# Kernel tuning notes

Hardware: AMD Instinct MI355X
Metric: run time of the kernel (lower is better)

The kernel has to match this reference:

```python
import jax, jax.numpy as jnp
import numpy as np

B, L, T, IN, H, OUT = 1024, 64, 128, 13, 64, 13
NEG = -1e30


def gru_step(x, h, Wih, Whh, bih, bhh):
    # PyTorch GRU cell: gates ordered (r, z, n)
    gi = x @ Wih.T + bih          # [B, 3H]
    gh = h @ Whh.T + bhh          # [B, 3H]
    ir, iz, inn = jnp.split(gi, 3, axis=-1)
    hr, hz, hn = jnp.split(gh, 3, axis=-1)
    r = jax.nn.sigmoid(ir + hr)
    z = jax.nn.sigmoid(iz + hz)
    n = jnp.tanh(inn + r * hn)
    return (1.0 - z) * n + z * h


def setup_inputs() -> dict:
    key = jax.random.key(0)
    ks = jax.random.split(key, 10)
    s = float(1.0 / np.sqrt(H))
    x = jax.random.normal(ks[0], (B, L, IN), jnp.float32)
    lengths = jax.random.randint(ks[1], (B,), 1, L + 1).at[0].set(L)
    Wih = jax.random.uniform(ks[2], (3 * H, IN), jnp.float32, -s, s)
    Whh = jax.random.uniform(ks[3], (3 * H, H), jnp.float32, -s, s)
    bih = jax.random.uniform(ks[4], (3 * H,), jnp.float32, -s, s)
    bhh = jax.random.uniform(ks[5], (3 * H,), jnp.float32, -s, s)
    Wf = jax.random.uniform(ks[6], (OUT, H), jnp.float32, -s, s)
    bf = jax.random.uniform(ks[7], (OUT,), jnp.float32, -s, s)
    Wa = jax.random.uniform(ks[8], (H, H), jnp.float32, -s, s)
    ba = jax.random.uniform(ks[9], (H,), jnp.float32, -s, s)
    return dict(x=x, lengths=lengths, output_length=T, Wih=Wih, Whh=Whh,
                bih=bih, bhh=bhh, Wf=Wf, bf=bf, Wa=Wa, ba=ba)


def reference(x, lengths, output_length, Wih, Whh, bih, bhh, Wf, bf, Wa, ba):
    b, l = x.shape[0], x.shape[1]
    xT = jnp.swapaxes(x, 0, 1)                        # [L, B, IN]
    h0 = jnp.zeros((b, H), x.dtype)

    # Encoder: masked GRU emulating pack_padded/pad_packed semantics:
    # hidden frozen past each sequence's length; outputs zero past length.
    def enc(h, inp):
        t, xt = inp
        hn = gru_step(xt, h, Wih, Whh, bih, bhh)
        valid = (t < lengths)[:, None]
        h = jnp.where(valid, hn, h)
        return h, jnp.where(valid, hn, 0.0)

    h, outs = jax.lax.scan(enc, h0, (jnp.arange(l), xT))
    # output[:, -1, :] of the padded output (zeros for seqs shorter than max)
    nin = outs[-1] @ Wf.T + bf                        # [B, OUT]

    Tn = output_length
    buf0 = jnp.zeros((Tn, b, H), x.dtype)             # growing past-prediction buffer

    def dec(carry, t):
        h, buf, nin = carry
        hn = gru_step(nin, h, Wih, Whh, bih, bhh)     # output_lstm == hidden (1 layer, 1 step)
        # attention recomputed over all past predictions (softmax over time axis)
        logits = jnp.einsum('tbh,gh->tbg', buf, Wa) + ba      # [T, B, H]
        logits = jnp.where((jnp.arange(Tn) < t)[:, None, None], logits, NEG)
        w = jax.nn.softmax(logits, axis=0)
        o = hn + jnp.sum(w * buf, axis=0)             # at t=0 buffer is all zeros -> +0
        y = o @ Wf.T + bf
        return (hn, buf.at[t].set(o), y), y

    _, ys = jax.lax.scan(dec, (h, buf0, nin), jnp.arange(Tn))
    return jnp.swapaxes(ys, 0, 1)                     # [B, T, OUT]
```

## Files before the change

kernel.cpp:

```cpp
#include <hip/hip_runtime.h>
#include <stdint.h>
#include <math.h>

#define BATCH 1024
#define SEQL  64
#define TDEC  128
#define NIN   13
#define NH    64
#define NOUT  13

typedef _Float16 h2 __attribute__((ext_vector_type(2)));
typedef __fp16   g2 __attribute__((ext_vector_type(2)));

union FU  { uint32_t u; float f; };
union HU  { uint16_t u; _Float16 h; };
union H2U { uint32_t u; h2 h; g2 g; };

__device__ __forceinline__ float bf2f(uint16_t v) { FU t; t.u = ((uint32_t)v) << 16; return t.f; }
__device__ __forceinline__ float hf2f(uint16_t v) { HU t; t.u = v; return (float)t.h; }

__device__ __forceinline__ float ldf(const void* p, long i, int mode) {
    if (mode == 1) return bf2f(((const uint16_t*)p)[i]);
    if (mode == 2) return hf2f(((const uint16_t*)p)[i]);
    return ((const float*)p)[i];
}

__device__ __forceinline__ bool pass_stats(const void* p, int n, int lane, int mode,
                                           float band_lo, float band_hi, float max_ok) {
    int m = (n + 1) / 2;
    int cnt = (m < 64) ? m : 64;
    bool ok_max = true, in_band = false;
    if (lane < cnt) {
        long pos = 2L * (((long)lane * m) / cnt);
        float v = (mode == 1) ? bf2f(((const uint16_t*)p)[pos])
                              : hf2f(((const uint16_t*)p)[pos]);
        float a = fabsf(v);
        ok_max  = (a <= max_ok);
        in_band = (a >= band_lo && a <= band_hi);
    }
    bool allmax = __all(ok_max);
    int nb = (int)__popcll(__ballot(in_band));
    int need = cnt / 4; if (need < 1) need = 1;
    return allmax && (nb >= need);
}
__device__ __forceinline__ int detect(const void* p, int n, int lane,
                                      float band_lo, float band_hi, float max_ok) {
    if (pass_stats(p, n, lane, 1, band_lo, band_hi, max_ok)) return 1;
    if (pass_stats(p, n, lane, 2, band_lo, band_hi, max_ok)) return 2;
    return 0;
}
__device__ __forceinline__ bool detect_len64(const int* p, int lane) {
    int v = p[2 * lane + 1];
    return __all(v == 0);
}

__device__ __forceinline__ float dot2(h2 a, h2 b, float c) {
#if __has_builtin(__builtin_amdgcn_fdot2)
    return __builtin_amdgcn_fdot2(a, b, c, false);
#else
    return c + (float)a[0] * (float)b[0] + (float)a[1] * (float)b[1];
#endif
}
__device__ __forceinline__ uint32_t pku(float a, float b) {
    H2U t; t.g = __builtin_amdgcn_cvt_pkrtz(a, b); return t.u;
}
__device__ __forceinline__ h2 uh(uint32_t u) { H2U t; t.u = u; return t.h; }
__device__ __forceinline__ float rcp_(float x) { return __builtin_amdgcn_rcpf(x); }
__device__ __forceinline__ float exp2_(float x) {
#if __has_builtin(__builtin_amdgcn_exp2f)
    return __builtin_amdgcn_exp2f(x);
#else
    return __expf(x * 0.69314718056f);
#endif
}
__device__ __forceinline__ float sigm2(float xs)  { return rcp_(1.0f + exp2_(-xs)); }
__device__ __forceinline__ float tanh2(float xs)  { return 1.0f - 2.0f * rcp_(exp2_(xs) + 1.0f); }
__device__ __forceinline__ void wb() { __builtin_amdgcn_wave_barrier(); }

__device__ __forceinline__ float swap1(float v) {
    FU a; a.f = v;
    FU b; b.u = (uint32_t)__builtin_amdgcn_mov_dpp((int)a.u, 0xB1, 0xF, 0xF, true);
    return b.f;
}

#define BWRITE(DSTB, V)                                                    \
    {                                                                      \
        float _w  = swap1(V);                                              \
        float _lo = odd ? _w  : (V);                                       \
        float _hi = odd ? (V) : _w;                                        \
        (DSTB)[jhalf] = pku(_lo, _hi);                                     \
    }

#define BREAD(SRC, DST)                                                    \
    {                                                                      \
        _Pragma("unroll")                                                  \
        for (int _k = 0; _k < 32; _k += 4) {                               \
            uint4 _q = *(const uint4*)((SRC) + _k);                        \
            (DST)[_k]     = _q.x; (DST)[_k + 1] = _q.y;                    \
            (DST)[_k + 2] = _q.z; (DST)[_k + 3] = _q.w;                    \
        }                                                                  \
    }

#define DEC_STEP(T_, HRD, HWR, OB_, YSLOT)                                         \
    {                                                                              \
        uint32_t hpk[32];                                                          \
        BREAD(HRD, hpk);                                                           \
        float arA = bcr, azA = bcz, hnA = bnh, anA = bni;                          \
        float arB = 0.0f, azB = 0.0f, hnB = 0.0f;                                  \
        float arC = 0.0f, azC = 0.0f, hnC = 0.0f;                                  \
        float arD = 0.0f, azD = 0.0f, hnD = 0.0f;                                  \
        _Pragma("unroll")                                                          \
        for (int k = 0; k < 32; k += 4) {                                          \
            h2 h0 = uh(hpk[k]), h1 = uh(hpk[k + 1]);                               \
            h2 h2v = uh(hpk[k + 2]), h3 = uh(hpk[k + 3]);                          \
            arA = dot2(whhr[k],     h0, arA); azA = dot2(whhz[k],     h0, azA); hnA = dot2(whhn[k],     h0, hnA); \
            arB = dot2(whhr[k + 1], h1, arB); azB = dot2(whhz[k + 1], h1, azB); hnB = dot2(whhn[k + 1], h1, hnB); \
            arC = dot2(whhr[k + 2], h2v, arC); azC = dot2(whhz[k + 2], h2v, azC); hnC = dot2(whhn[k + 2], h2v, hnC); \
            arD = dot2(whhr[k + 3], h3, arD); azD = dot2(whhz[k + 3], h3, azD); hnD = dot2(whhn[k + 3], h3, hnD); \
        }                                                                          \
        _Pragma("unroll")                                                          \
        for (int p = 0; p < 7; ++p) {                                              \
            h2 xv = uh(ypk[p]);                                                    \
            arB = dot2(wihr[p], xv, arB);                                          \
            azB = dot2(wihz[p], xv, azB);                                          \
            anA = dot2(wihn[p], xv, anA);                                          \
        }                                                                          \
        float ar = (arA + arB) + (arC + arD);                                      \
        float az = (azA + azB) + (azC + azD);                                      \
        float hna = (hnA + hnB) + (hnC + hnD);                                     \
        float r_ = sigm2(ar);                                                      \
        float z_ = sigm2(az);                                                      \
        float n_ = tanh2(anA + r_ * hna);                                          \
        float hnew = n_ + z_ * (h - n_);                                           \
        h = hnew;                                                                  \
        BWRITE(HWR, hnew);                                                         \
        float attn = ((T_) > 0) ? num * rcp_(Zs) : 0.0f;                           \
        float o_ = hnew + attn;                                                    \
        BWRITE(OB_, o_);                                                           \
        uint32_t opk[32];                                                          \
        BREAD(OB_, opk);                                                           \
        float sA = baj, yA = bfj, sB = 0.0f, yB = 0.0f;                            \
        float sC = 0.0f, yC = 0.0f, sD = 0.0f, yD = 0.0f;                          \
        _Pragma("unroll")                                                          \
        for (int k = 0; k < 32; k += 4) {                                          \
            h2 o0 = uh(opk[k]), o1 = uh(opk[k + 1]);                               \
            h2 o2 = uh(opk[k + 2]), o3 = uh(opk[k + 3]);                           \
            sA = dot2(wap[k],     o0, sA); yA = dot2(wfp[k],     o0, yA);          \
            sB = dot2(wap[k + 1], o1, sB); yB = dot2(wfp[k + 1], o1, yB);          \
            sC = dot2(wap[k + 2], o2, sC); yC = dot2(wfp[k + 2], o2, yC);          \
            sD = dot2(wap[k + 3], o3, sD); yD = dot2(wfp[k + 3], o3, yD);          \
        }                                                                          \
        float yv_ = (yA + yB) + (yC + yD);                                         \
        YSLOT = yv_;                                                               \
        float yz = (j < NOUT) ? yv_ : 0.0f;                                        \
        uint32_t pr_ = pku(yz, swap1(yz));                                         \
        _Pragma("unroll")                                                          \
        for (int k = 0; k < 7; ++k) ypk[k] = __builtin_amdgcn_readlane(pr_, 2 * k);\
        float s_  = (sA + sB) + (sC + sD);                                         \
        float mn = fmaxf(m, s_);                                                   \
        float al = exp2_(m - mn);                                                  \
        float pp = exp2_(s_ - mn);                                                 \
        Zs  = Zs * al + pp;                                                        \
        num = num * al + pp * o_;                                                  \
        m = mn;                                                                    \
    }

#define ENC_STEP(T_, HRD, HWR)                                                     \
    {                                                                              \
        uint32_t hpk[32];                                                          \
        BREAD(HRD, hpk);                                                           \
        uint4 q0 = *(const uint4*)(&xs2[(T_)][0]);                                 \
        uint4 q1 = *(const uint4*)(&xs2[(T_)][4]);                                 \
        float arA = bcr, azA = bcz, hnA = bnh, anA = bni;                          \
        float arB = 0.0f, azB = 0.0f, hnB = 0.0f;                                  \
        float arC = 0.0f, azC = 0.0f, hnC = 0.0f;                                  \
        float arD = 0.0f, azD = 0.0f, hnD = 0.0f;                                  \
        _Pragma("unroll")                                                          \
        for (int k = 0; k < 32; k += 4) {                                          \
            h2 h0 = uh(hpk[k]), h1 = uh(hpk[k + 1]);                               \
            h2 h2v = uh(hpk[k + 2]), h3 = uh(hpk[k + 3]);                          \
            arA = dot2(whhr[k],     h0, arA); azA = dot2(whhz[k],     h0, azA); hnA = dot2(whhn[k],     h0, hnA); \
            arB = dot2(whhr[k + 1], h1, arB); azB = dot2(whhz[k + 1], h1, azB); hnB = dot2(whhn[k + 1], h1, hnB); \
            arC = dot2(whhr[k + 2], h2v, arC); azC = dot2(whhz[k + 2], h2v, azC); hnC = dot2(whhn[k + 2], h2v, hnC); \
            arD = dot2(whhr[k + 3], h3, arD); azD = dot2(whhz[k + 3], h3, azD); hnD = dot2(whhn[k + 3], h3, hnD); \
        }                                                                          \
        {                                                                          \
            uint32_t xw[8] = {q0.x, q0.y, q0.z, q0.w, q1.x, q1.y, q1.z, q1.w};     \
            _Pragma("unroll")                                                      \
            for (int p = 0; p < 7; ++p) {                                          \
                h2 xv = uh(xw[p]);                                                 \
                arB = dot2(wihr[p], xv, arB);                                      \
                azB = dot2(wihz[p], xv, azB);                                      \
                anA = dot2(wihn[p], xv, anA);                                      \
            }                                                                      \
        }                                                                          \
        float ar = (arA + arB) + (arC + arD);                                      \
        float az = (azA + azB) + (azC + azD);                                      \
        float hna = (hnA + hnB) + (hnC + hnD);                                     \
        float r_ = sigm2(ar);                                                      \
        float z_ = sigm2(az);                                                      \
        float n_ = tanh2(anA + r_ * hna);                                          \
        float hnew = n_ + z_ * (h - n_);                                           \
        bool upd = ((T_) < len);                                                   \
        h = upd ? hnew : h;                                                        \
        if ((T_) == SEQL - 1) out_last = upd ? hnew : 0.0f;                        \
        BWRITE(HWR, h);                                                            \
    }

__global__ __launch_bounds__(64, 1)
void gru_attn_kernel(const void* __restrict__ x, const int* __restrict__ lengths,
                     const void* __restrict__ Wih, const void* __restrict__ Whh,
                     const void* __restrict__ bih, const void* __restrict__ bhh,
                     const void* __restrict__ Wf, const void* __restrict__ bfv,
                     const void* __restrict__ Wa, const void* __restrict__ ba,
                     float* __restrict__ out)
{
    const int b = blockIdx.x;
    const int j = threadIdx.x;
    const bool odd = j & 1;
    const int jhalf = j >> 1;

    __shared__ __align__(16) uint32_t xs2[SEQL][8];
    __shared__ __align__(16) uint32_t hb[2][32];
    __shared__ __align__(16) uint32_t ob[2][32];

    const int dX   = detect(x,   BATCH * SEQL * NIN, j, 0.25f, 4.0f, 16.0f);
    const int dWih = detect(Wih, 3 * NH * NIN, j, 0.04f, 0.13f, 0.14f);
    const int dWhh = detect(Whh, 3 * NH * NH,  j, 0.04f, 0.13f, 0.14f);
    const int dBih = detect(bih, 3 * NH,       j, 0.04f, 0.13f, 0.14f);
    const int dBhh = detect(bhh, 3 * NH,       j, 0.04f, 0.13f, 0.14f);
    const int dWf  = detect(Wf,  NOUT * NH,    j, 0.04f, 0.13f, 0.14f);
    const int dBf  = detect(bfv, NOUT,         j, 0.04f, 0.13f, 0.14f);
    const int dWa  = detect(Wa,  NH * NH,      j, 0.04f, 0.13f, 0.14f);
    const int dBa  = detect(ba,  NH,           j, 0.04f, 0.13f, 0.14f);
    const bool len64 = detect_len64(lengths, j);

    const float L2E  = 1.44269504089f;
    const float L2E2 = 2.88539008177f;

    h2 wihr[7], wihz[7], wihn[7];
    h2 whhr[32], whhz[32], whhn[32];
    h2 wap[32], wfp[32];

#pragma unroll
    for (int k = 0; k < 7; ++k) {
        float a0 = ldf(Wih, (0 * NH + j) * NIN + 2 * k, dWih);
        float a1 = (2 * k + 1 < NIN) ? ldf(Wih, (0 * NH + j) * NIN + 2 * k + 1, dWih) : 0.0f;
        wihr[k] = uh(pku(a0 * L2E, a1 * L2E));
        float b0 = ldf(Wih, (1 * NH + j) * NIN + 2 * k, dWih);
        float b1 = (2 * k + 1 < NIN) ? ldf(Wih, (1 * NH + j) * NIN + 2 * k + 1, dWih) : 0.0f;
        wihz[k] = uh(pku(b0 * L2E, b1 * L2E));
        float c0 = ldf(Wih, (2 * NH + j) * NIN + 2 * k, dWih);
        float c1 = (2 * k + 1 < NIN) ? ldf(Wih, (2 * NH + j) * NIN + 2 * k + 1, dWih) : 0.0f;
        wihn[k] = uh(pku(c0 * L2E2, c1 * L2E2));
    }
    const int jf = (j < NOUT) ? j : 0;
#pragma unroll
    for (int k = 0; k < 32; ++k) {
        whhr[k] = uh(pku(ldf(Whh, (0 * NH + j) * NH + 2 * k, dWhh) * L2E,
                         ldf(Whh, (0 * NH + j) * NH + 2 * k + 1, dWhh) * L2E));
        whhz[k] = uh(pku(ldf(Whh, (1 * NH + j) * NH + 2 * k, dWhh) * L2E,
                         ldf(Whh, (1 * NH + j) * NH + 2 * k + 1, dWhh) * L2E));
        whhn[k] = uh(pku(ldf(Whh, (2 * NH + j) * NH + 2 * k, dWhh) * L2E2,
                         ldf(Whh, (2 * NH + j) * NH + 2 * k + 1, dWhh) * L2E2));
        wap[k]  = uh(pku(ldf(Wa, j * NH + 2 * k, dWa) * L2E,
                         ldf(Wa, j * NH + 2 * k + 1, dWa) * L2E));
        wfp[k]  = uh(pku(ldf(Wf, jf * NH + 2 * k, dWf),
                         ldf(Wf, jf * NH + 2 * k + 1, dWf)));
    }

    const float bcr = (ldf(bih, j, dBih)      + ldf(bhh, j, dBhh))      * L2E;
    const float bcz = (ldf(bih, NH + j, dBih) + ldf(bhh, NH + j, dBhh)) * L2E;
    const float bni = ldf(bih, 2 * NH + j, dBih) * L2E2;
    const float bnh = ldf(bhh, 2 * NH + j, dBhh) * L2E2;
    const float baj = ldf(ba, j, dBa) * L2E;
    const float bfj = ldf(bfv, jf, dBf);
    const int len = len64 ? lengths[2 * b] : lengths[b];

    {
        const long base = ((long)b * SEQL + j) * NIN;
        float v[14];
#pragma unroll
        for (int k = 0; k < NIN; ++k) v[k] = ldf(x, base + k, dX);
        v[13] = 0.0f;
#pragma unroll
        for (int p = 0; p < 7; ++p) xs2[j][p] = pku(v[2 * p], v[2 * p + 1]);
        xs2[j][7] = 0u;
    }
    wb();

    float h = 0.0f;
    float out_last = 0.0f;

    BWRITE(&hb[0][0], 0.0f);

#pragma unroll 1
    for (int t0 = 0; t0 < SEQL; t0 += 2) {
        ENC_STEP(t0,     (&hb[0][0]), (&hb[1][0]));
        ENC_STEP(t0 + 1, (&hb[1][0]), (&hb[0][0]));
    }

    uint32_t ypk[7];
    {
        BWRITE(&ob[0][0], out_last);
        uint32_t opk[32];
        BREAD(&ob[0][0], opk);
        float nA = bfj, nB = 0.0f, nC = 0.0f, nD = 0.0f;
#pragma unroll
        for (int k = 0; k < 32; k += 4) {
            nA = dot2(wfp[k],     uh(opk[k]),     nA);
            nB = dot2(wfp[k + 1], uh(opk[k + 1]), nB);
            nC = dot2(wfp[k + 2], uh(opk[k + 2]), nC);
            nD = dot2(wfp[k + 3], uh(opk[k + 3]), nD);
        }
        float nv = (nA + nB) + (nC + nD);
        float nz = (j < NOUT) ? nv : 0.0f;
        uint32_t pr = pku(nz, swap1(nz));
#pragma unroll
        for (int k = 0; k < 7; ++k) ypk[k] = __builtin_amdgcn_readlane(pr, 2 * k);
    }

    float m = -1e30f, Zs = 0.0f, num = 0.0f;

#pragma unroll 1
    for (int t0 = 0; t0 < TDEC; t0 += 4) {
        float y0, y1, y2, y3;
        DEC_STEP(t0 + 0, (&hb[0][0]), (&hb[1][0]), (&ob[0][0]), y0);
        DEC_STEP(t0 + 1, (&hb[1][0]), (&hb[0][0]), (&ob[1][0]), y1);
        DEC_STEP(t0 + 2, (&hb[0][0]), (&hb[1][0]), (&ob[0][0]), y2);
        DEC_STEP(t0 + 3, (&hb[1][0]), (&hb[0][0]), (&ob[1][0]), y3);
        if (j < NOUT) {
            size_t base_ = ((size_t)b * TDEC + t0) * NOUT + j;
            out[base_]            = y0;
            out[base_ + NOUT]     = y1;
            out[base_ + 2 * NOUT] = y2;
            out[base_ + 3 * NOUT] = y3;
        }
    }
}

extern "C" void kernel_launch(void* const* d_in, const int* in_sizes, int n_in,
                              void* d_out, int out_size, void* d_ws, size_t ws_size,
                              hipStream_t stream) {
    (void)in_sizes; (void)n_in; (void)out_size; (void)d_ws; (void)ws_size;
    const void* x      = d_in[0];
    const int* lengths = (const int*)d_in[1];
    const void* Wih = d_in[3];
    const void* Whh = d_in[4];
    const void* bih = d_in[5];
    const void* bhh = d_in[6];
    const void* Wf  = d_in[7];
    const void* bf  = d_in[8];
    const void* Wa  = d_in[9];
    const void* ba  = d_in[10];
    float* out = (float*)d_out;

    gru_attn_kernel<<<dim3(BATCH), dim3(64), 0, stream>>>(
        x, lengths, Wih, Whh, bih, bhh, Wf, bf, Wa, ba, out);
}
```

Baseline: 210.3 us.

## Process two batch sequences per wavefront with interleaved independent recurrences

Each 64-lane block now handles two batch elements, interleaving the two independent GRU/attention recurrences so their dot-product chains can overlap and hide latency. This halves the grid to 512 blocks. Encoder inputs now stay in registers and are broadcast with readlane instead of being staged in shared memory. The cost is more register pressure and fewer blocks, which on a chip with many CUs may leave some units idle.

Result: slower. 308.4 us (+46.6%).

```diff
diff --git a/kernel.cpp b/kernel.cpp
--- a/kernel.cpp
+++ b/kernel.cpp
@@ -90,7 +90,6 @@
         float _hi = odd ? (V) : _w;                                        \
         (DSTB)[jhalf] = pku(_lo, _hi);                                     \
     }
-
 #define BREAD(SRC, DST)                                                    \
     {                                                                      \
         _Pragma("unroll")                                                  \
@@ -101,110 +100,73 @@
         }                                                                  \
     }
 
-#define DEC_STEP(T_, HRD, HWR, OB_, YSLOT)                                         \
-    {                                                                              \
-        uint32_t hpk[32];                                                          \
-        BREAD(HRD, hpk);                                                           \
-        float arA = bcr, azA = bcz, hnA = bnh, anA = bni;                          \
-        float arB = 0.0f, azB = 0.0f, hnB = 0.0f;                                  \
-        float arC = 0.0f, azC = 0.0f, hnC = 0.0f;                                  \
-        float arD = 0.0f, azD = 0.0f, hnD = 0.0f;                                  \
-        _Pragma("unroll")                                                          \
-        for (int k = 0; k < 32; k += 4) {                                          \
-            h2 h0 = uh(hpk[k]), h1 = uh(hpk[k + 1]);                               \
-            h2 h2v = uh(hpk[k + 2]), h3 = uh(hpk[k + 3]);                          \
-            arA = dot2(whhr[k],     h0, arA); azA = dot2(whhz[k],     h0, azA); hnA = dot2(whhn[k],     h0, hnA); \
-            arB = dot2(whhr[k + 1], h1, arB); azB = dot2(whhz[k + 1], h1, azB); hnB = dot2(whhn[k + 1], h1, hnB); \
-            arC = dot2(whhr[k + 2], h2v, arC); azC = dot2(whhz[k + 2], h2v, azC); hnC = dot2(whhn[k + 2], h2v, hnC); \
-            arD = dot2(whhr[k + 3], h3, arD); azD = dot2(whhz[k + 3], h3, azD); hnD = dot2(whhn[k + 3], h3, hnD); \
-        }                                                                          \
-        _Pragma("unroll")                                                          \
-        for (int p = 0; p < 7; ++p) {                                              \
-            h2 xv = uh(ypk[p]);                                                    \
-            arB = dot2(wihr[p], xv, arB);                                          \
-            azB = dot2(wihz[p], xv, azB);                                          \
-            anA = dot2(wihn[p], xv, anA);                                          \
-        }                                                                          \
-        float ar = (arA + arB) + (arC + arD);                                      \
-        float az = (azA + azB) + (azC + azD);                                      \
-        float hna = (hnA + hnB) + (hnC + hnD);                                     \
-        float r_ = sigm2(ar);                                                      \
-        float z_ = sigm2(az);                                                      \
-        float n_ = tanh2(anA + r_ * hna);                                          \
-        float hnew = n_ + z_ * (h - n_);                                           \
-        h = hnew;                                                                  \
-        BWRITE(HWR, hnew);                                                         \
-        float attn = ((T_) > 0) ? num * rcp_(Zs) : 0.0f;                           \
-        float o_ = hnew + attn;                                                    \
-        BWRITE(OB_, o_);                                                           \
-        uint32_t opk[32];                                                          \
-        BREAD(OB_, opk);                                                           \
-        float sA = baj, yA = bfj, sB = 0.0f, yB = 0.0f;                            \
-        float sC = 0.0f, yC = 0.0f, sD = 0.0f, yD = 0.0f;                          \
-        _Pragma("unroll")                                                          \
-        for (int k = 0; k < 32; k += 4) {                                          \
-            h2 o0 = uh(opk[k]), o1 = uh(opk[k + 1]);                               \
-            h2 o2 = uh(opk[k + 2]), o3 = uh(opk[k + 3]);                           \
-            sA = dot2(wap[k],     o0, sA); yA = dot2(wfp[k],     o0, yA);          \
-            sB = dot2(wap[k + 1], o1, sB); yB = dot2(wfp[k + 1], o1, yB);          \
-            sC = dot2(wap[k + 2], o2, sC); yC = dot2(wfp[k + 2], o2, yC);          \
-            sD = dot2(wap[k + 3], o3, sD); yD = dot2(wfp[k + 3], o3, yD);          \
-        }                                                                          \
-        float yv_ = (yA + yB) + (yC + yD);                                         \
-        YSLOT = yv_;                                                               \
-        float yz = (j < NOUT) ? yv_ : 0.0f;                                        \
-        uint32_t pr_ = pku(yz, swap1(yz));                                         \
-        _Pragma("unroll")                                                          \
-        for (int k = 0; k < 7; ++k) ypk[k] = __builtin_amdgcn_readlane(pr_, 2 * k);\
-        float s_  = (sA + sB) + (sC + sD);                                         \
-        float mn = fmaxf(m, s_);                                                   \
-        float al = exp2_(m - mn);                                                  \
-        float pp = exp2_(s_ - mn);                                                 \
-        Zs  = Zs * al + pp;                                                        \
-        num = num * al + pp * o_;                                                  \
-        m = mn;                                                                    \
-    }
-
-#define ENC_STEP(T_, HRD, HWR)                                                     \
-    {                                                                              \
-        uint32_t hpk[32];                                                          \
-        BREAD(HRD, hpk);                                                           \
-        uint4 q0 = *(const uint4*)(&xs2[(T_)][0]);                                 \
-        uint4 q1 = *(const uint4*)(&xs2[(T_)][4]);                                 \
-        float arA = bcr, azA = bcz, hnA = bnh, anA = bni;                          \
-        float arB = 0.0f, azB = 0.0f, hnB = 0.0f;                                  \
-        float arC = 0.0f, azC = 0.0f, hnC = 0.0f;                                  \
-        float arD = 0.0f, azD = 0.0f, hnD = 0.0f;                                  \
-        _Pragma("unroll")                                                          \
-        for (int k = 0; k < 32; k += 4) {                                          \
-            h2 h0 = uh(hpk[k]), h1 = uh(hpk[k + 1]);                               \
-            h2 h2v = uh(hpk[k + 2]), h3 = uh(hpk[k + 3]);                          \
-            arA = dot2(whhr[k],     h0, arA); azA = dot2(whhz[k],     h0, azA); hnA = dot2(whhn[k],     h0, hnA); \
-            arB = dot2(whhr[k + 1], h1, arB); azB = dot2(whhz[k + 1], h1, azB); hnB = dot2(whhn[k + 1], h1, hnB); \
-            arC = dot2(whhr[k + 2], h2v, arC); azC = dot2(whhz[k + 2], h2v, azC); hnC = dot2(whhn[k + 2], h2v, hnC); \
-            arD = dot2(whhr[k + 3], h3, arD); azD = dot2(whhz[k + 3], h3, azD); hnD = dot2(whhn[k + 3], h3, hnD); \
-        }                                                                          \
-        {                                                                          \
-            uint32_t xw[8] = {q0.x, q0.y, q0.z, q0.w, q1.x, q1.y, q1.z, q1.w};     \
-            _Pragma("unroll")                                                      \
-            for (int p = 0; p < 7; ++p) {                                          \
-                h2 xv = uh(xw[p]);                                                 \
-                arB = dot2(wihr[p], xv, arB);                                      \
-                azB = dot2(wihz[p], xv, azB);                                      \
-                anA = dot2(wihn[p], xv, anA);                                      \
-            }                                                                      \
-        }                                                                          \
-        float ar = (arA + arB) + (arC + arD);                                      \
-        float az = (azA + azB) + (azC + azD);                                      \
-        float hna = (hnA + hnB) + (hnC + hnD);                                     \
-        float r_ = sigm2(ar);                                                      \
-        float z_ = sigm2(az);                                                      \
-        float n_ = tanh2(anA + r_ * hna);                                          \
-        float hnew = n_ + z_ * (h - n_);                                           \
-        bool upd = ((T_) < len);                                                   \
-        h = upd ? hnew : h;                                                        \
-        if ((T_) == SEQL - 1) out_last = upd ? hnew : 0.0f;                        \
-        BWRITE(HWR, h);                                                            \
+#define DECL_ACC(S)                                                        \
+    float arA##S = bcr, azA##S = bcz, hnA##S = bnh, anA##S = bni;          \
+    float arB##S = 0.0f, azB##S = 0.0f, hnB##S = 0.0f;                     \
+    float arC##S = 0.0f, azC##S = 0.0f, hnC##S = 0.0f;                     \
+    float arD##S = 0.0f, azD##S = 0.0f, hnD##S = 0.0f;
+
+#define WHHQ(S, k)                                                         \
+    {                                                                      \
+        h2 q0 = uh(hpk##S[(k)]),     q1 = uh(hpk##S[(k) + 1]);             \
+        h2 q2 = uh(hpk##S[(k) + 2]), q3 = uh(hpk##S[(k) + 3]);             \
+        arA##S = dot2(whhr[(k)],     q0, arA##S); azA##S = dot2(whhz[(k)],     q0, azA##S); hnA##S = dot2(whhn[(k)],     q0, hnA##S); \
+        arB##S = dot2(whhr[(k) + 1], q1, arB##S); azB##S = dot2(whhz[(k) + 1], q1, azB##S); hnB##S = dot2(whhn[(k) + 1], q1, hnB##S); \
+        arC##S = dot2(whhr[(k) + 2], q2, arC##S); azC##S = dot2(whhz[(k) + 2], q2, azC##S); hnC##S = dot2(whhn[(k) + 2], q2, hnC##S); \
+        arD##S = dot2(whhr[(k) + 3], q3, arD##S); azD##S = dot2(whhz[(k) + 3], q3, azD##S); hnD##S = dot2(whhn[(k) + 3], q3, hnD##S); \
+    }
+
+#define WIHD(S, XW)                                                        \
+    _Pragma("unroll")                                                      \
+    for (int p = 0; p < 7; ++p) {                                          \
+        h2 xv = uh((XW)[p]);                                               \
+        arB##S = dot2(wihr[p], xv, arB##S);                                \
+        azB##S = dot2(wihz[p], xv, azB##S);                                \
+        anA##S = dot2(wihn[p], xv, anA##S);                                \
+    }
+
+#define GRU_TAIL(S)                                                        \
+    float hnew##S;                                                         \
+    {                                                                      \
+        float ar  = (arA##S + arB##S) + (arC##S + arD##S);                 \
+        float az  = (azA##S + azB##S) + (azC##S + azD##S);                 \
+        float hna = (hnA##S + hnB##S) + (hnC##S + hnD##S);                 \
+        float r_ = sigm2(ar);                                              \
+        float z_ = sigm2(az);                                              \
+        float n_ = tanh2(anA##S + r_ * hna);                               \
+        hnew##S = n_ + z_ * (hs##S - n_);                                  \
+    }
+
+#define DECL_SY(S)                                                         \
+    float sA##S = baj, sB##S = 0.0f, sC##S = 0.0f, sD##S = 0.0f;           \
+    float yA##S = bfj, yB##S = 0.0f, yC##S = 0.0f, yD##S = 0.0f;
+
+#define SYQ(S, k)                                                          \
+    {                                                                      \
+        h2 q0 = uh(opk##S[(k)]),     q1 = uh(opk##S[(k) + 1]);             \
+        h2 q2 = uh(opk##S[(k) + 2]), q3 = uh(opk##S[(k) + 3]);             \
+        sA##S = dot2(wap[(k)],     q0, sA##S); yA##S = dot2(wfp[(k)],     q0, yA##S); \
+        sB##S = dot2(wap[(k) + 1], q1, sB##S); yB##S = dot2(wfp[(k) + 1], q1, yB##S); \
+        sC##S = dot2(wap[(k) + 2], q2, sC##S); yC##S = dot2(wfp[(k) + 2], q2, yC##S); \
+        sD##S = dot2(wap[(k) + 3], q3, sD##S); yD##S = dot2(wfp[(k) + 3], q3, yD##S); \
+    }
+
+#define SMX(S)                                                             \
+    {                                                                      \
+        float mn = fmaxf(m##S, s_##S);                                     \
+        float al = exp2_(m##S - mn);                                       \
+        float pp = exp2_(s_##S - mn);                                      \
+        Zs##S  = Zs##S * al + pp;                                          \
+        num##S = num##S * al + pp * o_##S;                                 \
+        m##S = mn;                                                         \
+    }
+
+#define YPKU(S)                                                            \
+    {                                                                      \
+        float yz = (j < NOUT) ? yv##S : 0.0f;                              \
+        uint32_t pr = pku(yz, swap1(yz));                                  \
+        _Pragma("unroll")                                                  \
+        for (int k = 0; k < 7; ++k) ypk##S[k] = __builtin_amdgcn_readlane(pr, 2 * k); \
     }
 
 __global__ __launch_bounds__(64, 1)
@@ -215,13 +177,13 @@
                      const void* __restrict__ Wa, const void* __restrict__ ba,
                      float* __restrict__ out)
 {
-    const int b = blockIdx.x;
+    const int blk = blockIdx.x;
     const int j = threadIdx.x;
     const bool odd = j & 1;
     const int jhalf = j >> 1;
-
-    __shared__ __align__(16) uint32_t xs2[SEQL][8];
-    __shared__ __align__(16) uint32_t hb[2][32];
+    const int bA = 2 * blk, bB = 2 * blk + 1;
+
+    __shared__ __align__(16) uint32_t hb[2][2][32];
     __shared__ __align__(16) uint32_t ob[2][32];
 
     const int dX   = detect(x,   BATCH * SEQL * NIN, j, 0.25f, 4.0f, 16.0f);
@@ -275,66 +237,131 @@
     const float bnh = ldf(bhh, 2 * NH + j, dBhh) * L2E2;
     const float baj = ldf(ba, j, dBa) * L2E;
     const float bfj = ldf(bfv, jf, dBf);
-    const int len = len64 ? lengths[2 * b] : lengths[b];
-
+    const int len0 = len64 ? lengths[2 * bA] : lengths[bA];
+    const int len1 = len64 ? lengths[2 * bB] : lengths[bB];
+
+    uint32_t xp0[7], xp1[7];
     {
-        const long base = ((long)b * SEQL + j) * NIN;
-        float v[14];
-#pragma unroll
-        for (int k = 0; k < NIN; ++k) v[k] = ldf(x, base + k, dX);
-        v[13] = 0.0f;
-#pragma unroll
-        for (int p = 0; p < 7; ++p) xs2[j][p] = pku(v[2 * p], v[2 * p + 1]);
-        xs2[j][7] = 0u;
-    }
+        const long base0 = ((long)bA * SEQL + j) * NIN;
+        const long base1 = ((long)bB * SEQL + j) * NIN;
+        float v0[14], v1[14];
+#pragma unroll
+        for (int k = 0; k < NIN; ++k) { v0[k] = ldf(x, base0 + k, dX); v1[k] = ldf(x, base1 + k, dX); }
+        v0[13] = 0.0f; v1[13] = 0.0f;
+#pragma unroll
+        for (int p = 0; p < 7; ++p) {
+            xp0[p] = pku(v0[2 * p], v0[2 * p + 1]);
+            xp1[p] = pku(v1[2 * p], v1[2 * p + 1]);
+        }
+    }
+
+    float hs0 = 0.0f, hs1 = 0.0f;
+    float ol0 = 0.0f, ol1 = 0.0f;
+    int par = 0;
+
+    BWRITE(&hb[0][0][0], 0.0f);
+    BWRITE(&hb[0][1][0], 0.0f);
     wb();
 
-    float h = 0.0f;
-    float out_last = 0.0f;
-
-    BWRITE(&hb[0][0], 0.0f);
-
 #pragma unroll 1
-    for (int t0 = 0; t0 < SEQL; t0 += 2) {
-        ENC_STEP(t0,     (&hb[0][0]), (&hb[1][0]));
-        ENC_STEP(t0 + 1, (&hb[1][0]), (&hb[0][0]));
-    }
-
-    uint32_t ypk[7];
+    for (int t = 0; t < SEQL; ++t) {
+        uint32_t hpk0[32], hpk1[32];
+        BREAD(&hb[par][0][0], hpk0);
+        BREAD(&hb[par][1][0], hpk1);
+
+        uint32_t xw0[7], xw1[7];
+#pragma unroll
+        for (int p = 0; p < 7; ++p) {
+            xw0[p] = __builtin_amdgcn_readlane(xp0[p], t);
+            xw1[p] = __builtin_amdgcn_readlane(xp1[p], t);
+        }
+
+        DECL_ACC(0) DECL_ACC(1)
+#pragma unroll
+        for (int k = 0; k < 32; k += 4) { WHHQ(0, k) WHHQ(1, k) }
+        WIHD(0, xw0) WIHD(1, xw1)
+
+        GRU_TAIL(0) GRU_TAIL(1)
+        {
+            bool u0 = (t < len0), u1 = (t < len1);
+            hs0 = u0 ? hnew0 : hs0;
+            hs1 = u1 ? hnew1 : hs1;
+            if (t == SEQL - 1) { ol0 = u0 ? hnew0 : 0.0f; ol1 = u1 ? hnew1 : 0.0f; }
+        }
+        BWRITE(&hb[par ^ 1][0][0], hs0);
+        BWRITE(&hb[par ^ 1][1][0], hs1);
+        par ^= 1;
+    }
+
+    uint32_t ypk0[7], ypk1[7];
     {
-        BWRITE(&ob[0][0], out_last);
-        uint32_t opk[32];
-        BREAD(&ob[0][0], opk);
-        float nA = bfj, nB = 0.0f, nC = 0.0f, nD = 0.0f;
+        BWRITE(&ob[0][0], ol0);
+        BWRITE(&ob[1][0], ol1);
+        uint32_t opk0[32], opk1[32];
+        BREAD(&ob[0][0], opk0);
+        BREAD(&ob[1][0], opk1);
+        float n0A = bfj, n0B = 0.f, n0C = 0.f, n0D = 0.f;
+        float n1A = bfj, n1B = 0.f, n1C = 0.f, n1D = 0.f;
 #pragma unroll
         for (int k = 0; k < 32; k += 4) {
-            nA = dot2(wfp[k],     uh(opk[k]),     nA);
-            nB = dot2(wfp[k + 1], uh(opk[k + 1]), nB);
-            nC = dot2(wfp[k + 2], uh(opk[k + 2]), nC);
-            nD = dot2(wfp[k + 3], uh(opk[k + 3]), nD);
-        }
-        float nv = (nA + nB) + (nC + nD);
-        float nz = (j < NOUT) ? nv : 0.0f;
-        uint32_t pr = pku(nz, swap1(nz));
-#pragma unroll
-        for (int k = 0; k < 7; ++k) ypk[k] = __builtin_amdgcn_readlane(pr, 2 * k);
-    }
-
-    float m = -1e30f, Zs = 0.0f, num = 0.0f;
+            n0A = dot2(wfp[k],     uh(opk0[k]),     n0A);
+            n1A = dot2(wfp[k],     uh(opk1[k]),     n1A);
+            n0B = dot2(wfp[k + 1], uh(opk0[k + 1]), n0B);
+            n1B = dot2(wfp[k + 1], uh(opk1[k + 1]), n1B);
+            n0C = dot2(wfp[k + 2], uh(opk0[k + 2]), n0C);
+            n1C = dot2(wfp[k + 2], uh(opk1[k + 2]), n1C);
+            n0D = dot2(wfp[k + 3], uh(opk0[k + 3]), n0D);
+            n1D = dot2(wfp[k + 3], uh(opk1[k + 3]), n1D);
+        }
+        float yv0 = (n0A + n0B) + (n0C + n0D);
+        float yv1 = (n1A + n1B) + (n1C + n1D);
+        YPKU(0) YPKU(1)
+    }
+
+    float m0 = -1e30f, Zs0 = 0.0f, num0 = 0.0f;
+    float m1 = -1e30f, Zs1 = 0.0f, num1 = 0.0f;
 
 #pragma unroll 1
-    for (int t0 = 0; t0 < TDEC; t0 += 4) {
-        float y0, y1, y2, y3;
-        DEC_STEP(t0 + 0, (&hb[0][0]), (&hb[1][0]), (&ob[0][0]), y0);
-        DEC_STEP(t0 + 1, (&hb[1][0]), (&hb[0][0]), (&ob[1][0]), y1);
-        DEC_STEP(t0 + 2, (&hb[0][0]), (&hb[1][0]), (&ob[0][0]), y2);
-        DEC_STEP(t0 + 3, (&hb[1][0]), (&hb[0][0]), (&ob[1][0]), y3);
+    for (int t = 0; t < TDEC; ++t) {
+        uint32_t hpk0[32], hpk1[32];
+        BREAD(&hb[par][0][0], hpk0);
+        BREAD(&hb[par][1][0], hpk1);
+
+        DECL_ACC(0) DECL_ACC(1)
+#pragma unroll
+        for (int k = 0; k < 32; k += 4) { WHHQ(0, k) WHHQ(1, k) }
+        WIHD(0, ypk0) WIHD(1, ypk1)
+
+        GRU_TAIL(0) GRU_TAIL(1)
+        hs0 = hnew0;
+        hs1 = hnew1;
+        BWRITE(&hb[par ^ 1][0][0], hs0);
+        BWRITE(&hb[par ^ 1][1][0], hs1);
+        par ^= 1;
+
+        float o_0 = hs0 + ((t > 0) ? num0 * rcp_(Zs0) : 0.0f);
+        float o_1 = hs1 + ((t > 0) ? num1 * rcp_(Zs1) : 0.0f);
+        BWRITE(&ob[0][0], o_0);
+        BWRITE(&ob[1][0], o_1);
+        uint32_t opk0[32], opk1[32];
+        BREAD(&ob[0][0], opk0);
+        BREAD(&ob[1][0], opk1);
+
+        DECL_SY(0) DECL_SY(1)
+#pragma unroll
+        for (int k = 0; k < 32; k += 4) { SYQ(0, k) SYQ(1, k) }
+
+        float s_0 = (sA0 + sB0) + (sC0 + sD0);
+        float s_1 = (sA1 + sB1) + (sC1 + sD1);
+        float yv0 = (yA0 + yB0) + (yC0 + yD0);
+        float yv1 = (yA1 + yB1) + (yC1 + yD1);
+
+        SMX(0) SMX(1)
+        YPKU(0) YPKU(1)
+
         if (j < NOUT) {
-            size_t base_ = ((size_t)b * TDEC + t0) * NOUT + j;
-            out[base_]            = y0;
-            out[base_ + NOUT]     = y1;
-            out[base_ + 2 * NOUT] = y2;
-            out[base_ + 3 * NOUT] = y3;
+            out[((size_t)bA * TDEC + t) * NOUT + j] = yv0;
+            out[((size_t)bB * TDEC + t) * NOUT + j] = yv1;
         }
     }
 }
@@ -355,6 +382,6 @@
     const void* ba  = d_in[10];
     float* out = (float*)d_out;
 
-    gru_attn_kernel<<<dim3(BATCH), dim3(64), 0, stream>>>(
+    gru_attn_kernel<<<dim3(BATCH / 2), dim3(64), 0, stream>>>(
         x, lengths, Wih, Whh, bih, bhh, Wf, bf, Wa, ba, out);
 }
```
